# Kernel tuning notes

Measured on AMD Instinct MI355X. Metric: run time of the kernel, lower is better.

Reference implementation:

```python
import jax, jax.numpy as jnp
import numpy as np

IN_F, OUT_F, RANK, ALPHA = 4096, 4096, 8, 32.0

def setup_inputs() -> dict:
    key = jax.random.key(0)
    kx, kw, ka, kb, kbias = jax.random.split(key, 5)
    x = jax.random.normal(kx, (4, 2048, IN_F), dtype=jnp.float32)
    weight = jax.random.normal(kw, (OUT_F, IN_F), dtype=jnp.float32) * 0.02
    a = jax.random.normal(ka, (OUT_F, RANK), dtype=jnp.float32) * 0.02
    b = jax.random.normal(kb, (RANK, IN_F), dtype=jnp.float32) * 0.02  # zeros in init; use randn for nontrivial test
    bias = jax.random.normal(kbias, (OUT_F,), dtype=jnp.float32) * 0.02
    return {"x": x, "weight": weight, "a": a, "b": b, "bias": bias}

def reference(x, weight, a, b, bias):
    # F.linear(x, W, bias) + F.linear(x, a @ b) * alpha / r
    base = jnp.einsum('bsi,oi->bso', x, weight) + bias
    # low-rank path computed in factored form (same math as x @ (a@b).T)
    lora = jnp.einsum('bsr,or->bso', jnp.einsum('bsi,ri->bsr', x, b), a)
    return base + lora * (ALPHA / RANK)
```

## Files before the change

### kernel.cpp

```cpp
#include <hip/hip_runtime.h>
#include <stdint.h>

#define IN_F 4096
#define OUT_F 4096
#define M_TOT 8192
#define LORA_SCALE 4.0f

typedef unsigned short u16;
typedef __attribute__((ext_vector_type(8))) short bf16x8;
typedef __attribute__((ext_vector_type(4))) float f32x4;

__device__ __forceinline__ u16 f2bf(float f) {
  union { float f; unsigned u; } v; v.f = f;
  unsigned r = v.u + 0x7FFFu + ((v.u >> 16) & 1u);
  return (u16)(r >> 16);
}

__device__ __forceinline__ void gload_lds16(const void* g, void* l) {
  __builtin_amdgcn_global_load_lds(
      (const __attribute__((address_space(1))) void*)g,
      (__attribute__((address_space(3))) void*)l, 16, 0, 0);
}

__global__ void prep(const float* __restrict__ X, const float* __restrict__ W,
                     const float* __restrict__ A, const float* __restrict__ B,
                     u16* __restrict__ Xb, u16* __restrict__ Wb) {
  int bid = blockIdx.x;
  if (bid < 16384) {
    size_t base = ((size_t)bid * blockDim.x + threadIdx.x) * 8;
    const f32x4* p = (const f32x4*)(X + base);
    f32x4 v0 = __builtin_nontemporal_load(p);
    f32x4 v1 = __builtin_nontemporal_load(p + 1);
    uint4 pk;
    pk.x = (unsigned)f2bf(v0.x) | ((unsigned)f2bf(v0.y) << 16);
    pk.y = (unsigned)f2bf(v0.z) | ((unsigned)f2bf(v0.w) << 16);
    pk.z = (unsigned)f2bf(v1.x) | ((unsigned)f2bf(v1.y) << 16);
    pk.w = (unsigned)f2bf(v1.z) | ((unsigned)f2bf(v1.w) << 16);
    *(uint4*)(Xb + base) = pk;
  } else {
    int idx = (bid - 16384) * blockDim.x + threadIdx.x;
    int o  = idx >> 10;
    int i0 = (idx & 1023) << 2;
    const f32x4 w = __builtin_nontemporal_load((const f32x4*)(W + (size_t)o * IN_F + i0));
    float a0 = w.x, a1 = w.y, a2 = w.z, a3 = w.w;
#pragma unroll
    for (int r = 0; r < 8; ++r) {
      float ar = A[o * 8 + r] * LORA_SCALE;
      const float4 bv = *(const float4*)(B + (size_t)r * IN_F + i0);
      a0 += ar * bv.x; a1 += ar * bv.y; a2 += ar * bv.z; a3 += ar * bv.w;
    }
    uint2 pk;
    pk.x = (unsigned)f2bf(a0) | ((unsigned)f2bf(a1) << 16);
    pk.y = (unsigned)f2bf(a2) | ((unsigned)f2bf(a3) << 16);
    *(uint2*)(Wb + (size_t)o * IN_F + i0) = pk;
  }
}


#define ABASE(b) ((b) * 32768)
#define BBASE(b) ((b) * 32768 + 16384)

#define STAGE_A(b, h, kt) do { \
  gload_lds16(aG + (size_t)((h) * 128) * IN_F + (kt),      lds + ABASE(b) + ((h) * 128) * 64      + tid * 8); \
  gload_lds16(aG + (size_t)((h) * 128 + 64) * IN_F + (kt), lds + ABASE(b) + ((h) * 128 + 64) * 64 + tid * 8); \
} while (0)

#define STAGE_B(b, h, kt) do { \
  gload_lds16(bG + (size_t)((h) * 128) * IN_F + (kt),      lds + BBASE(b) + ((h) * 128) * 64      + tid * 8); \
  gload_lds16(bG + (size_t)((h) * 128 + 64) * IN_F + (kt), lds + BBASE(b) + ((h) * 128 + 64) * 64 + tid * 8); \
} while (0)

#define WAIT4 asm volatile("s_waitcnt vmcnt(4)" ::: "memory")
#define WAIT0 asm volatile("s_waitcnt vmcnt(0)" ::: "memory")

#define PHASE(b, p, STAGE_STMT) do { \
  __builtin_amdgcn_s_barrier(); \
  __builtin_amdgcn_sched_barrier(0); \
  if ((p) == 0) { \
    _Pragma("unroll") \
    for (int n = 0; n < 4; ++n) { \
      Bf0[n] = *(const bf16x8*)(lds + BBASE(b) + (rB + n * 16) * 64 + ck0); \
      Bf1[n] = *(const bf16x8*)(lds + BBASE(b) + (rB + n * 16) * 64 + ck1); \
    } \
  } \
  bf16x8 a00 = *(const bf16x8*)(lds + ABASE(b) + (rA + (2 * (p)) * 16) * 64 + ck0); \
  bf16x8 a01 = *(const bf16x8*)(lds + ABASE(b) + (rA + (2 * (p)) * 16) * 64 + ck1); \
  bf16x8 a10 = *(const bf16x8*)(lds + ABASE(b) + (rA + (2 * (p) + 1) * 16) * 64 + ck0); \
  bf16x8 a11 = *(const bf16x8*)(lds + ABASE(b) + (rA + (2 * (p) + 1) * 16) * 64 + ck1); \
  STAGE_STMT; \
  __builtin_amdgcn_s_setprio(1); \
  _Pragma("unroll") \
  for (int n = 0; n < 4; ++n) { \
    acc[2 * (p)][n]     = __builtin_amdgcn_mfma_f32_16x16x32_bf16(a00, Bf0[n], acc[2 * (p)][n], 0, 0, 0); \
    acc[2 * (p) + 1][n] = __builtin_amdgcn_mfma_f32_16x16x32_bf16(a10, Bf0[n], acc[2 * (p) + 1][n], 0, 0, 0); \
  } \
  _Pragma("unroll") \
  for (int n = 0; n < 4; ++n) { \
    acc[2 * (p)][n]     = __builtin_amdgcn_mfma_f32_16x16x32_bf16(a01, Bf1[n], acc[2 * (p)][n], 0, 0, 0); \
    acc[2 * (p) + 1][n] = __builtin_amdgcn_mfma_f32_16x16x32_bf16(a11, Bf1[n], acc[2 * (p) + 1][n], 0, 0, 0); \
  } \
  __builtin_amdgcn_s_setprio(0); \
} while (0)

__global__ __launch_bounds__(512, 2) void gemm8(const u16* __restrict__ Xb,
                                                const u16* __restrict__ Wb,
                                                const float* __restrict__ bias,
                                                float* __restrict__ out) {
  extern __shared__ u16 lds[];

  const int tid  = threadIdx.x;
  const int lane = tid & 63;
  const int wid  = tid >> 6;
  const int wr = wid >> 2, wc = wid & 3;
  const int lr = lane & 15, kg = lane >> 4;

  const int bid = blockIdx.x;
  const int swz = (bid & 7) * 64 + (bid >> 3);
  const int mt = swz >> 4, nt = swz & 15;
  const int m0 = mt * 256, n0 = nt * 256;

  const int srow = tid >> 3;
  const int swc  = (tid & 7) ^ (srow & 7);
  const u16* aG = Xb + (size_t)(m0 + srow) * IN_F + swc * 8;
  const u16* bG = Wb + (size_t)(n0 + srow) * IN_F + swc * 8;

  const int rA = wr * 128 + lr;
  const int rB = wc * 64 + lr;
  const int ck0 = ((kg) ^ (lane & 7)) * 8;
  const int ck1 = ((4 + kg) ^ (lane & 7)) * 8;

  f32x4 acc[8][4] = {};
  bf16x8 Bf0[4], Bf1[4];

  STAGE_B(0, 0, 0); STAGE_B(0, 1, 0);
  STAGE_A(0, 0, 0); STAGE_A(0, 1, 0);
  STAGE_B(1, 0, 64); STAGE_B(1, 1, 64);
  WAIT4;

  for (int i = 0; i < 31; ++i) {
    const int kt1 = i * 128 + 64, kt2 = i * 128 + 128, kt3 = i * 128 + 192;
    PHASE(0, 0, STAGE_A(1, 0, kt1));
    PHASE(0, 1, STAGE_A(1, 1, kt1));
    PHASE(0, 2, STAGE_B(0, 0, kt2));
    PHASE(0, 3, STAGE_B(0, 1, kt2));
    WAIT4;
    PHASE(1, 0, STAGE_A(0, 0, kt2));
    PHASE(1, 1, STAGE_A(0, 1, kt2));
    PHASE(1, 2, STAGE_B(1, 0, kt3));
    PHASE(1, 3, STAGE_B(1, 1, kt3));
    WAIT4;
  }
  PHASE(0, 0, STAGE_A(1, 0, 4032));
  PHASE(0, 1, STAGE_A(1, 1, 4032));
  PHASE(0, 2, );
  PHASE(0, 3, );
  WAIT0;
  PHASE(1, 0, );
  PHASE(1, 1, );
  PHASE(1, 2, );
  PHASE(1, 3, );

  float bv[4];
#pragma unroll
  for (int n = 0; n < 4; ++n) bv[n] = bias[n0 + wc * 64 + n * 16 + lr];
  const int rbase = m0 + wr * 128 + kg * 4;
#pragma unroll
  for (int m = 0; m < 8; ++m)
#pragma unroll
    for (int n = 0; n < 4; ++n) {
      int col = n0 + wc * 64 + n * 16 + lr;
#pragma unroll
      for (int r = 0; r < 4; ++r)
        __builtin_nontemporal_store(acc[m][n][r] + bv[n],
                                    &out[(size_t)(rbase + m * 16 + r) * OUT_F + col]);
    }
}

__global__ __launch_bounds__(256) void gemm_bias(const u16* __restrict__ Xb,
                                                 const u16* __restrict__ Wb,
                                                 const float* __restrict__ bias,
                                                 float* __restrict__ out) {
  __shared__ __align__(16) u16 ldsA[128 * 64];
  __shared__ __align__(16) u16 ldsB[128 * 64];

  const int tid  = threadIdx.x;
  const int wid  = tid >> 6;
  const int lane = tid & 63;
  const int nt = blockIdx.x & 31;
  const int mt = blockIdx.x >> 5;
  const int m0 = mt * 128, n0 = nt * 128;
  const int wr = wid >> 1, wc = wid & 1;
  const int lr = lane & 15;
  const int kg = lane >> 4;

  const int srow   = wid * 8 + (lane >> 3);
  const int schunk = (lane & 7) ^ (srow & 7);
  const u16* aSrc = Xb + (size_t)(m0 + srow) * IN_F + schunk * 8;
  const u16* bSrc = Wb + (size_t)(n0 + srow) * IN_F + schunk * 8;

  f32x4 acc[4][4] = {};

  for (int kt = 0; kt < IN_F; kt += 64) {
    __syncthreads();
#pragma unroll
    for (int j = 0; j < 4; ++j) {
      gload_lds16(aSrc + (size_t)(j * 32) * IN_F + kt, &ldsA[j * 2048 + wid * 512]);
      gload_lds16(bSrc + (size_t)(j * 32) * IN_F + kt, &ldsB[j * 2048 + wid * 512]);
    }
    __syncthreads();

#pragma unroll
    for (int s = 0; s < 2; ++s) {
      bf16x8 af[4], bfr[4];
#pragma unroll
      for (int m = 0; m < 4; ++m) {
        int r = wr * 64 + m * 16 + lr;
        int c = (s * 4 + kg) ^ (r & 7);
        af[m] = *(const bf16x8*)&ldsA[r * 64 + c * 8];
      }
#pragma unroll
      for (int n = 0; n < 4; ++n) {
        int r = wc * 64 + n * 16 + lr;
        int c = (s * 4 + kg) ^ (r & 7);
        bfr[n] = *(const bf16x8*)&ldsB[r * 64 + c * 8];
      }
#pragma unroll
      for (int m = 0; m < 4; ++m)
#pragma unroll
        for (int n = 0; n < 4; ++n)
          acc[m][n] = __builtin_amdgcn_mfma_f32_16x16x32_bf16(af[m], bfr[n], acc[m][n], 0, 0, 0);
    }
  }

  float bv[4];
#pragma unroll
  for (int n = 0; n < 4; ++n) bv[n] = bias[n0 + wc * 64 + n * 16 + lr];
  const int rbase = m0 + wr * 64 + kg * 4;
#pragma unroll
  for (int m = 0; m < 4; ++m)
#pragma unroll
    for (int n = 0; n < 4; ++n) {
      int col = n0 + wc * 64 + n * 16 + lr;
#pragma unroll
      for (int r = 0; r < 4; ++r)
        out[(size_t)(rbase + m * 16 + r) * OUT_F + col] = acc[m][n][r] + bv[n];
    }
}

__global__ void lora_t(const float* __restrict__ x, const float* __restrict__ B,
                       float* __restrict__ t) {
  int m = blockIdx.x;
  int tid = threadIdx.x, lane = tid & 63;
  float p[8] = {0, 0, 0, 0, 0, 0, 0, 0};
  for (int k = tid; k < IN_F; k += 256) {
    float xv = x[(size_t)m * IN_F + k];
#pragma unroll
    for (int r = 0; r < 8; ++r) p[r] += xv * B[r * IN_F + k];
  }
#pragma unroll
  for (int r = 0; r < 8; ++r) {
    float v = p[r];
    for (int off = 32; off; off >>= 1) v += __shfl_down(v, off);
    if (lane == 0) atomicAdd(&t[m * 8 + r], v);
  }
}

__global__ void fb_gemm(const float* __restrict__ x, const float* __restrict__ W,
                        const float* __restrict__ A, const float* __restrict__ bias,
                        const float* __restrict__ t, float* __restrict__ out) {
  __shared__ float sx[64][17];
  __shared__ float sw[64][17];
  int tx = threadIdx.x, ty = threadIdx.y;
  int tid = ty * 16 + tx;
  int m0 = blockIdx.y * 64, n0 = blockIdx.x * 64;
  float acc[4][4] = {};
  for (int kt = 0; kt < IN_F; kt += 16) {
    __syncthreads();
#pragma unroll
    for (int q = 0; q < 4; ++q) {
      int idx = q * 256 + tid;
      int r = idx >> 4, c = idx & 15;
      sx[r][c] = x[(size_t)(m0 + r) * IN_F + kt + c];
      sw[r][c] = W[(size_t)(n0 + r) * IN_F + kt + c];
    }
    __syncthreads();
#pragma unroll
    for (int k = 0; k < 16; ++k) {
      float xv[4], wv[4];
#pragma unroll
      for (int i = 0; i < 4; ++i) xv[i] = sx[ty * 4 + i][k];
#pragma unroll
      for (int j = 0; j < 4; ++j) wv[j] = sw[tx * 4 + j][k];
#pragma unroll
      for (int i = 0; i < 4; ++i)
#pragma unroll
        for (int j = 0; j < 4; ++j) acc[i][j] += xv[i] * wv[j];
    }
  }
#pragma unroll
  for (int i = 0; i < 4; ++i) {
    int m = m0 + ty * 4 + i;
    float tv[8];
#pragma unroll
    for (int r = 0; r < 8; ++r) tv[r] = t[m * 8 + r];
#pragma unroll
    for (int j = 0; j < 4; ++j) {
      int o = n0 + tx * 4 + j;
      float lora = 0.f;
#pragma unroll
      for (int r = 0; r < 8; ++r) lora += tv[r] * A[o * 8 + r];
      out[(size_t)m * OUT_F + o] = acc[i][j] + bias[o] + LORA_SCALE * lora;
    }
  }
}

extern "C" void kernel_launch(void* const* d_in, const int* in_sizes, int n_in,
                              void* d_out, int out_size, void* d_ws, size_t ws_size,
                              hipStream_t stream) {
  const float* x    = (const float*)d_in[0];
  const float* W    = (const float*)d_in[1];
  const float* A    = (const float*)d_in[2];
  const float* B    = (const float*)d_in[3];
  const float* bias = (const float*)d_in[4];
  float* out = (float*)d_out;

  const size_t xb_elems = (size_t)M_TOT * IN_F;
  const size_t wb_elems = (size_t)OUT_F * IN_F;
  const size_t need = (xb_elems + wb_elems) * sizeof(u16);

  if (ws_size >= need) {
    u16* Xb = (u16*)d_ws;
    u16* Wb = Xb + xb_elems;
    prep<<<32768, 256, 0, stream>>>(x, W, A, B, Xb, Wb);

    hipError_t e = hipFuncSetAttribute((const void*)gemm8,
                                       hipFuncAttributeMaxDynamicSharedMemorySize,
                                       131072);
    bool used8 = false;
    if (e == hipSuccess) {
      gemm8<<<512, 512, 131072, stream>>>(Xb, Wb, bias, out);
      used8 = (hipGetLastError() == hipSuccess);
    }
    if (!used8) {
      gemm_bias<<<(M_TOT / 128) * (OUT_F / 128), 256, 0, stream>>>(Xb, Wb, bias, out);
    }
  } else {
    float* t = (float*)d_ws;
    (void)hipMemsetAsync(t, 0, (size_t)M_TOT * 8 * sizeof(float), stream);
    lora_t<<<M_TOT, 256, 0, stream>>>(x, B, t);
    fb_gemm<<<dim3(OUT_F / 64, M_TOT / 64), dim3(16, 16), 0, stream>>>(x, W, A, bias, t, out);
  }
}
```

Measured before the change: 294.7 us.

## Switch main GEMM inner loop to 32x32x16 bf16 MFMA tiles

Replaces the 16x16x32 MFMA micro-tiles in gemm8 with 32x32x16 MFMA instructions. Each wave still covers a 128x64 output tile, now as 4x2 blocks of 32x32. The LDS fragment addressing, k-chunk swizzle indices and epilogue row/column mapping are changed to match the new register layout. Larger MFMAs mean fewer instructions and fewer LDS fragment reads per FLOP. An extra lgkmcnt drain between phases adds a sync point that may reduce overlap.

```diff
diff --git a/kernel.cpp b/kernel.cpp
--- a/kernel.cpp
+++ b/kernel.cpp
@@ -9,6 +9,7 @@
 typedef unsigned short u16;
 typedef __attribute__((ext_vector_type(8))) short bf16x8;
 typedef __attribute__((ext_vector_type(4))) float f32x4;
+typedef __attribute__((ext_vector_type(16))) float f32x16;
 
 __device__ __forceinline__ u16 f2bf(float f) {
   union { float f; unsigned u; } v; v.f = f;
@@ -72,33 +73,34 @@
 
 #define WAIT4 asm volatile("s_waitcnt vmcnt(4)" ::: "memory")
 #define WAIT0 asm volatile("s_waitcnt vmcnt(0)" ::: "memory")
-
-#define PHASE(b, p, STAGE_STMT) do { \
+#define DRAIN asm volatile("s_waitcnt lgkmcnt(0)" ::: "memory")
+
+#define MFMA32 __builtin_amdgcn_mfma_f32_32x32x16_bf16
+
+#define PHASE32(b, p, STAGE_STMT) do { \
   __builtin_amdgcn_s_barrier(); \
   __builtin_amdgcn_sched_barrier(0); \
+  bf16x8 a0 = *(const bf16x8*)(lds + ABASE(b) + (rA +  0) * 64 + ck[p]); \
+  bf16x8 a1 = *(const bf16x8*)(lds + ABASE(b) + (rA + 32) * 64 + ck[p]); \
+  bf16x8 a2 = *(const bf16x8*)(lds + ABASE(b) + (rA + 64) * 64 + ck[p]); \
+  bf16x8 a3 = *(const bf16x8*)(lds + ABASE(b) + (rA + 96) * 64 + ck[p]); \
   if ((p) == 0) { \
     _Pragma("unroll") \
-    for (int n = 0; n < 4; ++n) { \
-      Bf0[n] = *(const bf16x8*)(lds + BBASE(b) + (rB + n * 16) * 64 + ck0); \
-      Bf1[n] = *(const bf16x8*)(lds + BBASE(b) + (rB + n * 16) * 64 + ck1); \
+    for (int s = 0; s < 4; ++s) { \
+      bb0[s] = *(const bf16x8*)(lds + BBASE(b) + rB * 64 + ck[s]); \
+      bb1[s] = *(const bf16x8*)(lds + BBASE(b) + (rB + 32) * 64 + ck[s]); \
     } \
   } \
-  bf16x8 a00 = *(const bf16x8*)(lds + ABASE(b) + (rA + (2 * (p)) * 16) * 64 + ck0); \
-  bf16x8 a01 = *(const bf16x8*)(lds + ABASE(b) + (rA + (2 * (p)) * 16) * 64 + ck1); \
-  bf16x8 a10 = *(const bf16x8*)(lds + ABASE(b) + (rA + (2 * (p) + 1) * 16) * 64 + ck0); \
-  bf16x8 a11 = *(const bf16x8*)(lds + ABASE(b) + (rA + (2 * (p) + 1) * 16) * 64 + ck1); \
   STAGE_STMT; \
   __builtin_amdgcn_s_setprio(1); \
-  _Pragma("unroll") \
-  for (int n = 0; n < 4; ++n) { \
-    acc[2 * (p)][n]     = __builtin_amdgcn_mfma_f32_16x16x32_bf16(a00, Bf0[n], acc[2 * (p)][n], 0, 0, 0); \
-    acc[2 * (p) + 1][n] = __builtin_amdgcn_mfma_f32_16x16x32_bf16(a10, Bf0[n], acc[2 * (p) + 1][n], 0, 0, 0); \
-  } \
-  _Pragma("unroll") \
-  for (int n = 0; n < 4; ++n) { \
-    acc[2 * (p)][n]     = __builtin_amdgcn_mfma_f32_16x16x32_bf16(a01, Bf1[n], acc[2 * (p)][n], 0, 0, 0); \
-    acc[2 * (p) + 1][n] = __builtin_amdgcn_mfma_f32_16x16x32_bf16(a11, Bf1[n], acc[2 * (p) + 1][n], 0, 0, 0); \
-  } \
+  acc[0][0] = MFMA32(a0, bb0[p], acc[0][0], 0, 0, 0); \
+  acc[1][0] = MFMA32(a1, bb0[p], acc[1][0], 0, 0, 0); \
+  acc[2][0] = MFMA32(a2, bb0[p], acc[2][0], 0, 0, 0); \
+  acc[3][0] = MFMA32(a3, bb0[p], acc[3][0], 0, 0, 0); \
+  acc[0][1] = MFMA32(a0, bb1[p], acc[0][1], 0, 0, 0); \
+  acc[1][1] = MFMA32(a1, bb1[p], acc[1][1], 0, 0, 0); \
+  acc[2][1] = MFMA32(a2, bb1[p], acc[2][1], 0, 0, 0); \
+  acc[3][1] = MFMA32(a3, bb1[p], acc[3][1], 0, 0, 0); \
   __builtin_amdgcn_s_setprio(0); \
 } while (0)
 
@@ -112,7 +114,7 @@
   const int lane = tid & 63;
   const int wid  = tid >> 6;
   const int wr = wid >> 2, wc = wid & 3;
-  const int lr = lane & 15, kg = lane >> 4;
+  const int l31 = lane & 31, khi = lane >> 5;
 
   const int bid = blockIdx.x;
   const int swz = (bid & 7) * 64 + (bid >> 3);
@@ -124,13 +126,15 @@
   const u16* aG = Xb + (size_t)(m0 + srow) * IN_F + swc * 8;
   const u16* bG = Wb + (size_t)(n0 + srow) * IN_F + swc * 8;
 
-  const int rA = wr * 128 + lr;
-  const int rB = wc * 64 + lr;
-  const int ck0 = ((kg) ^ (lane & 7)) * 8;
-  const int ck1 = ((4 + kg) ^ (lane & 7)) * 8;
-
-  f32x4 acc[8][4] = {};
-  bf16x8 Bf0[4], Bf1[4];
+  const int rA = wr * 128 + l31;
+  const int rB = wc * 64 + l31;
+  const int ck[4] = { ((0 + khi) ^ (lane & 7)) * 8,
+                      ((2 + khi) ^ (lane & 7)) * 8,
+                      ((4 + khi) ^ (lane & 7)) * 8,
+                      ((6 + khi) ^ (lane & 7)) * 8 };
+
+  f32x16 acc[4][2] = {};
+  bf16x8 bb0[4], bb1[4];
 
   STAGE_B(0, 0, 0); STAGE_B(0, 1, 0);
   STAGE_A(0, 0, 0); STAGE_A(0, 1, 0);
@@ -139,40 +143,42 @@
 
   for (int i = 0; i < 31; ++i) {
     const int kt1 = i * 128 + 64, kt2 = i * 128 + 128, kt3 = i * 128 + 192;
-    PHASE(0, 0, STAGE_A(1, 0, kt1));
-    PHASE(0, 1, STAGE_A(1, 1, kt1));
-    PHASE(0, 2, STAGE_B(0, 0, kt2));
-    PHASE(0, 3, STAGE_B(0, 1, kt2));
+    PHASE32(0, 0, STAGE_A(1, 0, kt1));
+    PHASE32(0, 1, STAGE_A(1, 1, kt1));
+    DRAIN;
+    PHASE32(0, 2, STAGE_B(0, 0, kt2));
+    PHASE32(0, 3, STAGE_B(0, 1, kt2));
     WAIT4;
-    PHASE(1, 0, STAGE_A(0, 0, kt2));
-    PHASE(1, 1, STAGE_A(0, 1, kt2));
-    PHASE(1, 2, STAGE_B(1, 0, kt3));
-    PHASE(1, 3, STAGE_B(1, 1, kt3));
+    PHASE32(1, 0, STAGE_A(0, 0, kt2));
+    PHASE32(1, 1, STAGE_A(0, 1, kt2));
+    DRAIN;
+    PHASE32(1, 2, STAGE_B(1, 0, kt3));
+    PHASE32(1, 3, STAGE_B(1, 1, kt3));
     WAIT4;
   }
-  PHASE(0, 0, STAGE_A(1, 0, 4032));
-  PHASE(0, 1, STAGE_A(1, 1, 4032));
-  PHASE(0, 2, );
-  PHASE(0, 3, );
+  PHASE32(0, 0, STAGE_A(1, 0, 4032));
+  PHASE32(0, 1, STAGE_A(1, 1, 4032));
+  PHASE32(0, 2, );
+  PHASE32(0, 3, );
   WAIT0;
-  PHASE(1, 0, );
-  PHASE(1, 1, );
-  PHASE(1, 2, );
-  PHASE(1, 3, );
-
-  float bv[4];
-#pragma unroll
-  for (int n = 0; n < 4; ++n) bv[n] = bias[n0 + wc * 64 + n * 16 + lr];
-  const int rbase = m0 + wr * 128 + kg * 4;
-#pragma unroll
-  for (int m = 0; m < 8; ++m)
-#pragma unroll
-    for (int n = 0; n < 4; ++n) {
-      int col = n0 + wc * 64 + n * 16 + lr;
-#pragma unroll
-      for (int r = 0; r < 4; ++r)
-        __builtin_nontemporal_store(acc[m][n][r] + bv[n],
-                                    &out[(size_t)(rbase + m * 16 + r) * OUT_F + col]);
+  PHASE32(1, 0, );
+  PHASE32(1, 1, );
+  PHASE32(1, 2, );
+  PHASE32(1, 3, );
+
+  const float bv0 = bias[n0 + wc * 64 + l31];
+  const float bv1 = bias[n0 + wc * 64 + 32 + l31];
+  const size_t colbase = (size_t)n0 + wc * 64 + l31;
+  const int rowbase = m0 + wr * 128 + 4 * khi;
+#pragma unroll
+  for (int mb = 0; mb < 4; ++mb)
+#pragma unroll
+    for (int reg = 0; reg < 16; ++reg) {
+      int row = rowbase + mb * 32 + (reg & 3) + 8 * (reg >> 2);
+      __builtin_nontemporal_store(acc[mb][0][reg] + bv0,
+                                  &out[(size_t)row * OUT_F + colbase]);
+      __builtin_nontemporal_store(acc[mb][1][reg] + bv1,
+                                  &out[(size_t)row * OUT_F + colbase + 32]);
     }
 }
 
```

Result: slower. 317.0 us (+7.6%).
